# Kernel tuning notes

Measured on AMD Instinct MI355X. Metric: run time of the kernel, lower is better.

Reference implementation:

```python
import jax, jax.numpy as jnp
import numpy as np

D_MODEL = 1024
N_HEADS = 16
D_HEAD = D_MODEL // N_HEADS


def setup_inputs() -> dict:
    key = jax.random.key(0)
    ks = jax.random.split(key, 5)
    B, T = 2, 2048
    x = jax.random.normal(ks[0], (B, T, D_MODEL), dtype=jnp.float32)
    s = 1.0 / np.sqrt(D_MODEL)
    W_qkv = jax.random.normal(ks[1], (D_MODEL, 3 * D_MODEL), dtype=jnp.float32) * s
    b_qkv = jnp.zeros((3 * D_MODEL,), dtype=jnp.float32)
    W_proj = jax.random.normal(ks[2], (D_MODEL, D_MODEL), dtype=jnp.float32) * s
    b_proj = jnp.zeros((D_MODEL,), dtype=jnp.float32)
    return {"x": x, "W_qkv": W_qkv, "b_qkv": b_qkv, "W_proj": W_proj, "b_proj": b_proj}


def reference(x, W_qkv, b_qkv, W_proj, b_proj):
    B, T, C = x.shape
    qkv = x @ W_qkv + b_qkv                      # [B,T,3C]
    q, k, v = jnp.split(qkv, 3, axis=-1)
    # [B,T,C] -> [B,H,T,Dh]
    def to_heads(t):
        return t.reshape(B, T, N_HEADS, D_HEAD).transpose(0, 2, 1, 3)
    q, k, v = to_heads(q), to_heads(k), to_heads(v)
    scale = 1.0 / np.sqrt(D_HEAD).astype(np.float32)
    scores = jnp.einsum('bhqd,bhkd->bhqk', q, k) * scale  # [B,H,T,T]
    causal = jnp.tril(jnp.ones((T, T), dtype=bool))
    scores = jnp.where(causal, scores, -jnp.inf)
    attn = jax.nn.softmax(scores, axis=-1)
    out = jnp.einsum('bhqk,bhkd->bhqd', attn, v)          # [B,H,T,Dh]
    out = out.transpose(0, 2, 1, 3).reshape(B, T, C)
    return out @ W_proj + b_proj
```

## Files before the change

kernel.cpp:

```cpp
#include <hip/hip_runtime.h>
#include <hip/hip_bf16.h>
#include <cstdint>


using u16 = unsigned short;
using u32 = unsigned int;

typedef __bf16 bf16x8 __attribute__((ext_vector_type(8)));
typedef float f32x4 __attribute__((ext_vector_type(4)));

#define AS1 __attribute__((address_space(1)))
#define AS3 __attribute__((address_space(3)))

__device__ __forceinline__ u16 f2bf(float f) {
  u32 u = __float_as_uint(f);
  u += 0x7fffu + ((u >> 16) & 1u);
  return (u16)(u >> 16);
}
__device__ __forceinline__ u32 pack2bf(float a, float b) {
  u32 ua = __float_as_uint(a) + 0x8000u;
  u32 ub = __float_as_uint(b) + 0x8000u;
  return (ua >> 16) | (ub & 0xffff0000u);
}

__global__ __launch_bounds__(256) void prep(const float* __restrict__ x,
                                            u16* __restrict__ xb,
                                            const float* __restrict__ W0,
                                            u16* __restrict__ T0,
                                            const float* __restrict__ W1,
                                            u16* __restrict__ T1) {
  const int bx = blockIdx.x;
  const int tid = threadIdx.x;
  if (bx < 4096) {
    const int i = bx * 256 + tid;
    float4 v = ((const float4*)x)[i];
    ushort4 o;
    o.x = f2bf(v.x); o.y = f2bf(v.y); o.z = f2bf(v.z); o.w = f2bf(v.w);
    ((ushort4*)xb)[i] = o;
    return;
  }
  __shared__ float t[32][33];
  const int idx = bx - 4096;
  const int bxx = idx & 127, by = idx >> 7;
  const float* W; u16* Wt; int N, n0;
  if (bxx < 96) { W = W0; Wt = T0; N = 3072; n0 = bxx * 32; }
  else          { W = W1; Wt = T1; N = 1024; n0 = (bxx - 96) * 32; }
  const int k0 = by * 32;
  const int tx = tid & 31, ty = tid >> 5;
#pragma unroll
  for (int i = 0; i < 4; ++i)
    t[ty + i * 8][tx] = W[(size_t)(k0 + ty + i * 8) * N + n0 + tx];
  __syncthreads();
#pragma unroll
  for (int i = 0; i < 4; ++i)
    Wt[(size_t)(n0 + ty + i * 8) * 1024 + k0 + tx] = f2bf(t[tx][ty + i * 8]);
}

#define MFMA16 __builtin_amdgcn_mfma_f32_16x16x32_bf16

__global__ __launch_bounds__(512, 2) void gemm_qkv(const u16* __restrict__ A,
                                                   const u16* __restrict__ Bt,
                                                   const float* __restrict__ bias,
                                                   u16* __restrict__ qb,
                                                   u16* __restrict__ KF,
                                                   u16* __restrict__ VF,
                                                   float sc_val) {
  constexpr int NT = 16;
  __shared__ __align__(16) u16 sm[2 * 4 * 8192];

  const int tid  = threadIdx.x;
  const int lane = tid & 63;
  const int w    = tid >> 6;
  const int quad = lane >> 4;
  const int l15  = lane & 15;

  const int bid = blockIdx.x;
  const int xcd = bid & 7, c = bid >> 3;
  const int mt = (xcd >> 1) * 4 + (c & 3);
  const int nt = (xcd & 1) * 6 + (c >> 2);
  const int bm = mt * 256, bn = nt * 256;

  const int wr = (w >> 2) * 128;
  const int wc = (w & 3) * 64;

  const int rowS = w * 8 + (lane >> 3);
  const int scol = (((lane & 7) ^ (lane >> 3)) << 3);

#define STAGE(matp, rowbase, ldsoff, ktile)                                     \
  do {                                                                          \
    const u16* _s = (matp) + ((size_t)((rowbase) + rowS) << 10) +               \
                    ((ktile) << 6) + scol;                                      \
    u16* _d = sm + (ldsoff) + (w << 9);                                         \
    __builtin_amdgcn_global_load_lds((AS1 const void*)_s, (AS3 void*)_d,        \
                                     16, 0, 0);                                 \
    __builtin_amdgcn_global_load_lds((AS1 const void*)(_s + (64 << 10)),        \
                                     (AS3 void*)(_d + 4096), 16, 0, 0);         \
  } while (0)

  const int raoff = (wr >> 7) * 8192;
  const int rboff = (2 + (wc >> 7)) * 8192;
  const int av0 = l15 * 64 + ((quad ^ (l15 & 7)) << 3);
  const int av1 = l15 * 64 + (((4 + quad) ^ (l15 & 7)) << 3);
  const int bv0 = ((wc & 64) + l15) * 64 + ((quad ^ (l15 & 7)) << 3);
  const int bv1 = ((wc & 64) + l15) * 64 + (((4 + quad) ^ (l15 & 7)) << 3);

  STAGE(A,  bm,       0 * 8192, 0);
  STAGE(A,  bm + 128, 1 * 8192, 0);
  STAGE(Bt, bn,       2 * 8192, 0);
  STAGE(Bt, bn + 128, 3 * 8192, 0);
  STAGE(Bt, bn,       32768 + 2 * 8192, 1);
  STAGE(A,  bm,       32768 + 0 * 8192, 1);
  STAGE(A,  bm + 128, 32768 + 1 * 8192, 1);
  asm volatile("s_waitcnt vmcnt(6)" ::: "memory");
  __builtin_amdgcn_s_barrier();

  f32x4 acc[8][4] = {};
  bf16x8 a[4][2], b[4][2];

#pragma unroll 2
  for (int kt = 0; kt < NT; ++kt) {
    const int bo  = (kt & 1) * 32768;
    const int nbo = bo ^ 32768;
    const u16* smA = sm + bo + raoff;
    const u16* smB = sm + bo + rboff;

#pragma unroll
    for (int mi = 0; mi < 4; ++mi) {
      a[mi][0] = *(const bf16x8*)(smA + mi * 1024 + av0);
      a[mi][1] = *(const bf16x8*)(smA + mi * 1024 + av1);
    }
#pragma unroll
    for (int ni = 0; ni < 2; ++ni) {
      b[ni][0] = *(const bf16x8*)(smB + ni * 1024 + bv0);
      b[ni][1] = *(const bf16x8*)(smB + ni * 1024 + bv1);
    }
    if (kt + 1 < NT) STAGE(Bt, bn + 128, nbo + 3 * 8192, kt + 1);
    __builtin_amdgcn_s_barrier();
    asm volatile("s_waitcnt lgkmcnt(0)" ::: "memory");
    __builtin_amdgcn_s_setprio(1);
#pragma unroll
    for (int mi = 0; mi < 4; ++mi)
#pragma unroll
      for (int ni = 0; ni < 2; ++ni) {
        acc[mi][ni] = MFMA16(a[mi][0], b[ni][0], acc[mi][ni], 0, 0, 0);
        acc[mi][ni] = MFMA16(a[mi][1], b[ni][1], acc[mi][ni], 0, 0, 0);
      }
    __builtin_amdgcn_s_setprio(0);
    __builtin_amdgcn_s_barrier();

#pragma unroll
    for (int ni = 2; ni < 4; ++ni) {
      b[ni][0] = *(const bf16x8*)(smB + ni * 1024 + bv0);
      b[ni][1] = *(const bf16x8*)(smB + ni * 1024 + bv1);
    }
    __builtin_amdgcn_s_barrier();
    asm volatile("s_waitcnt lgkmcnt(0)" ::: "memory");
    __builtin_amdgcn_s_setprio(1);
#pragma unroll
    for (int mi = 0; mi < 4; ++mi)
#pragma unroll
      for (int ni = 2; ni < 4; ++ni) {
        acc[mi][ni] = MFMA16(a[mi][0], b[ni][0], acc[mi][ni], 0, 0, 0);
        acc[mi][ni] = MFMA16(a[mi][1], b[ni][1], acc[mi][ni], 0, 0, 0);
      }
    __builtin_amdgcn_s_setprio(0);
    __builtin_amdgcn_s_barrier();

#pragma unroll
    for (int mi = 0; mi < 4; ++mi) {
      a[mi][0] = *(const bf16x8*)(smA + (4 + mi) * 1024 + av0);
      a[mi][1] = *(const bf16x8*)(smA + (4 + mi) * 1024 + av1);
    }
    if (kt + 2 < NT) STAGE(Bt, bn, bo + 2 * 8192, kt + 2);
    __builtin_amdgcn_s_barrier();
    asm volatile("s_waitcnt lgkmcnt(0)" ::: "memory");
    __builtin_amdgcn_s_setprio(1);
#pragma unroll
    for (int mi = 0; mi < 4; ++mi)
#pragma unroll
      for (int ni = 2; ni < 4; ++ni) {
        acc[4 + mi][ni] = MFMA16(a[mi][0], b[ni][0], acc[4 + mi][ni], 0, 0, 0);
        acc[4 + mi][ni] = MFMA16(a[mi][1], b[ni][1], acc[4 + mi][ni], 0, 0, 0);
      }
    __builtin_amdgcn_s_setprio(0);
    __builtin_amdgcn_s_barrier();

    if (kt + 2 < NT) {
      STAGE(A, bm,       bo + 0 * 8192, kt + 2);
      STAGE(A, bm + 128, bo + 1 * 8192, kt + 2);
    }
    __builtin_amdgcn_s_barrier();
    __builtin_amdgcn_s_setprio(1);
#pragma unroll
    for (int mi = 0; mi < 4; ++mi)
#pragma unroll
      for (int ni = 0; ni < 2; ++ni) {
        acc[4 + mi][ni] = MFMA16(a[mi][0], b[ni][0], acc[4 + mi][ni], 0, 0, 0);
        acc[4 + mi][ni] = MFMA16(a[mi][1], b[ni][1], acc[4 + mi][ni], 0, 0, 0);
      }
    __builtin_amdgcn_s_setprio(0);
    if (kt + 2 < NT)
      asm volatile("s_waitcnt vmcnt(6)" ::: "memory");
    else
      asm volatile("s_waitcnt vmcnt(0)" ::: "memory");
    __builtin_amdgcn_s_barrier();
  }
#undef STAGE

  const int crow0 = bm + wr + (quad << 2);
  const int ccol0 = bn + wc + l15;
  if (bn < 1024) {
#pragma unroll
    for (int ni = 0; ni < 4; ++ni) {
      const int n = ccol0 + ni * 16;
      const float bv = bias[n];
#pragma unroll
      for (int mi = 0; mi < 8; ++mi) {
        const int m0 = crow0 + mi * 16;
#pragma unroll
        for (int r = 0; r < 4; ++r)
          qb[(size_t)(m0 + r) * 1024 + n] = f2bf((acc[mi][ni][r] + bv) * sc_val);
      }
    }
  } else if (bn < 2048) {
#pragma unroll
    for (int ni = 0; ni < 4; ++ni) {
      const int n  = ccol0 + ni * 16;
      const int hk = (n - 1024) >> 6;
      const int d  = (n - 1024) & 63;
      const int hh = d >> 5, qd = (d >> 3) & 3, j = d & 7;
      const float bv = bias[n];
#pragma unroll
      for (int mi = 0; mi < 8; ++mi) {
#pragma unroll
        for (int r = 0; r < 4; ++r) {
          const int t  = crow0 + mi * 16 + r;
          const int bb = t >> 11, tt = t & 2047;
          const int kt = tt >> 6, mm = (tt >> 4) & 3, l = tt & 15;
          KF[((size_t)((bb * 16 + hk) * 32 + kt) * 8 + mm * 2 + hh) * 512 +
             (qd * 16 + l) * 8 + j] = f2bf(acc[mi][ni][r] + bv);
        }
      }
    }
  } else {
#pragma unroll
    for (int ni = 0; ni < 4; ++ni) {
      const int n  = ccol0 + ni * 16;
      const int hv = (n - 2048) >> 6;
      const int d  = (n - 2048) & 63;
      const int di = d >> 4, l = d & 15;
      const float bv = bias[n];
#pragma unroll
      for (int mi = 0; mi < 8; ++mi) {
#pragma unroll
        for (int r = 0; r < 4; ++r) {
          const int t  = crow0 + mi * 16 + r;
          const int bb = t >> 11, tt = t & 2047;
          const int kt = tt >> 6, to = tt & 63;
          const int mq = to >> 4, qd2 = (to >> 2) & 3, rr = to & 3;
          const int hh = mq >> 1, j = (mq & 1) * 4 + rr;
          VF[((size_t)((bb * 16 + hv) * 32 + kt) * 8 + hh * 4 + di) * 512 +
             (qd2 * 16 + l) * 8 + j] = f2bf(acc[mi][ni][r] + bv);
        }
      }
    }
  }
}

__global__ __launch_bounds__(256) void gemm_proj(const u16* __restrict__ A,
                                                 const u16* __restrict__ Bt,
                                                 const float* __restrict__ bias,
                                                 float* __restrict__ C) {
  constexpr int BM = 128, BN = 64, BK = 32;
  constexpr int K = 1024, N = 1024;
  __shared__ __align__(16) u16 lA[BM * BK];
  __shared__ __align__(16) u16 lB[BN * BK];
  const int tid  = threadIdx.x;
  const int lane = tid & 63;
  const int wave = tid >> 6;
  const int bm = blockIdx.x * BM;
  const int bn = blockIdx.y * BN;
  const int wr = wave * 32;

  f32x4 acc[2][4] = {};

  const int f0 = (wave << 10) + (lane << 4);
  const int f1 = f0 + 4096;
  const int ar0 = f0 >> 6, ac0 = (f0 & 63) >> 1;
  const int ar1 = f1 >> 6, ac1 = (f1 & 63) >> 1;

  const int arow = wr + (lane & 15);
  const int brow = (lane & 15);
  const int kk   = (lane >> 4) << 3;

  for (int k0 = 0; k0 < K; k0 += BK) {
    __builtin_amdgcn_global_load_lds((AS1 const void*)(A + (size_t)(bm + ar0) * K + k0 + ac0),
                                     (AS3 void*)(lA + (wave << 9)), 16, 0, 0);
    __builtin_amdgcn_global_load_lds((AS1 const void*)(A + (size_t)(bm + ar1) * K + k0 + ac1),
                                     (AS3 void*)(lA + ((wave + 4) << 9)), 16, 0, 0);
    __builtin_amdgcn_global_load_lds((AS1 const void*)(Bt + (size_t)(bn + ar0) * K + k0 + ac0),
                                     (AS3 void*)(lB + (wave << 9)), 16, 0, 0);
    __syncthreads();

    bf16x8 af[2], bfr[4];
#pragma unroll
    for (int mi = 0; mi < 2; ++mi)
      af[mi] = *(const bf16x8*)&lA[(arow + mi * 16) * BK + kk];
#pragma unroll
    for (int ni = 0; ni < 4; ++ni)
      bfr[ni] = *(const bf16x8*)&lB[(brow + ni * 16) * BK + kk];
#pragma unroll
    for (int mi = 0; mi < 2; ++mi)
#pragma unroll
      for (int ni = 0; ni < 4; ++ni)
        acc[mi][ni] = __builtin_amdgcn_mfma_f32_16x16x32_bf16(af[mi], bfr[ni],
                                                              acc[mi][ni], 0, 0, 0);
    __syncthreads();
  }

  const int crow0 = bm + wr + ((lane >> 4) << 2);
  const int ccol0 = bn + (lane & 15);
#pragma unroll
  for (int ni = 0; ni < 4; ++ni) {
    const int n = ccol0 + ni * 16;
    const float bv = bias[n];
#pragma unroll
    for (int mi = 0; mi < 2; ++mi) {
      const int m0 = crow0 + mi * 16;
#pragma unroll
      for (int r = 0; r < 4; ++r)
        C[(size_t)(m0 + r) * N + n] = acc[mi][ni][r] + bv;
    }
  }
}

__global__ __launch_bounds__(256) void attn_bal(const u16* __restrict__ qb,
                                                const u16* __restrict__ KF,
                                                const u16* __restrict__ VF,
                                                u16* __restrict__ out) {
  const int u  = blockIdx.x;
  const int bh = blockIdx.y;
  const int b = bh >> 4, h = bh & 15;
  const int tid = threadIdx.x;
  const int lane = tid & 63;
  const int w    = tid >> 6;
  const int quad = lane >> 4;
  const int l15  = lane & 15;
  const int g32 = (w & 1) ? (63 - u) : u;
  const int par = w >> 1;
  const int q0 = g32 * 32;
  const int ktmax = g32 >> 1;

  __shared__ float CB[2][64][35];

  const u16* qbase = qb + (size_t)b * 2048 * 1024 + h * 64;
  bf16x8 qf[2][2];
#pragma unroll
  for (int g = 0; g < 2; ++g)
#pragma unroll
    for (int hh = 0; hh < 2; ++hh)
      qf[g][hh] = *(const bf16x8*)(qbase + (size_t)(q0 + g * 16 + l15) * 1024 +
                                   hh * 32 + quad * 8);

  const size_t fb = (size_t)bh * 32 * 4096 + lane * 8;
  const u16* kfb = KF + fb;
  const u16* vfb = VF + fb;

  f32x4 accO[2][4] = {};
  float lrow[2] = {0.f, 0.f};

  bf16x8 kcur[4][2];
  {
    const u16* kp = kfb + (size_t)par * 4096;
#pragma unroll
    for (int m = 0; m < 4; ++m)
#pragma unroll
      for (int hh = 0; hh < 2; ++hh)
        kcur[m][hh] = *(const bf16x8*)(kp + (m * 2 + hh) * 512);
  }

  for (int kt = par; kt <= ktmax; kt += 2) {
    const u16* vp = vfb + (size_t)kt * 4096;
    bf16x8 vfr[2][4];
#pragma unroll
    for (int hh = 0; hh < 2; ++hh)
#pragma unroll
      for (int di = 0; di < 4; ++di)
        vfr[hh][di] = *(const bf16x8*)(vp + (hh * 4 + di) * 512);
    const int ktn = (kt + 2 <= ktmax) ? kt + 2 : ktmax;
    const u16* kpn = kfb + (size_t)ktn * 4096;
    bf16x8 knx[4][2];
#pragma unroll
    for (int m = 0; m < 4; ++m)
#pragma unroll
      for (int hh = 0; hh < 2; ++hh)
        knx[m][hh] = *(const bf16x8*)(kpn + (m * 2 + hh) * 512);

    const bool diag = (kt == ktmax);
    bf16x8 ap[2][2];
#pragma unroll
    for (int g = 0; g < 2; ++g) {
      f32x4 sT[4] = {};
#pragma unroll
      for (int m = 0; m < 4; ++m) {
        sT[m] = __builtin_amdgcn_mfma_f32_16x16x32_bf16(kcur[m][0], qf[g][0], sT[m], 0, 0, 0);
        sT[m] = __builtin_amdgcn_mfma_f32_16x16x32_bf16(kcur[m][1], qf[g][1], sT[m], 0, 0, 0);
      }
      float pv[4][4];
      if (diag) {
        const int qgl = q0 + g * 16 + l15;
#pragma unroll
        for (int m = 0; m < 4; ++m)
#pragma unroll
          for (int r = 0; r < 4; ++r) {
            const bool msk = (kt * 64 + m * 16 + quad * 4 + r) > qgl;
            pv[m][r] = msk ? 0.f : __builtin_amdgcn_exp2f(sT[m][r]);
          }
      } else {
#pragma unroll
        for (int m = 0; m < 4; ++m)
#pragma unroll
          for (int r = 0; r < 4; ++r)
            pv[m][r] = __builtin_amdgcn_exp2f(sT[m][r]);
      }
      const float s0 = (pv[0][0] + pv[0][1]) + (pv[0][2] + pv[0][3]);
      const float s1 = (pv[1][0] + pv[1][1]) + (pv[1][2] + pv[1][3]);
      const float s2 = (pv[2][0] + pv[2][1]) + (pv[2][2] + pv[2][3]);
      const float s3 = (pv[3][0] + pv[3][1]) + (pv[3][2] + pv[3][3]);
      lrow[g] += (s0 + s1) + (s2 + s3);

      union { u32 u4[4]; bf16x8 v; } t0, t1;
      t0.u4[0] = pack2bf(pv[0][0], pv[0][1]);
      t0.u4[1] = pack2bf(pv[0][2], pv[0][3]);
      t0.u4[2] = pack2bf(pv[1][0], pv[1][1]);
      t0.u4[3] = pack2bf(pv[1][2], pv[1][3]);
      t1.u4[0] = pack2bf(pv[2][0], pv[2][1]);
      t1.u4[1] = pack2bf(pv[2][2], pv[2][3]);
      t1.u4[2] = pack2bf(pv[3][0], pv[3][1]);
      t1.u4[3] = pack2bf(pv[3][2], pv[3][3]);
      ap[g][0] = t0.v;
      ap[g][1] = t1.v;
    }

#pragma unroll
    for (int hh = 0; hh < 2; ++hh)
#pragma unroll
      for (int di = 0; di < 4; ++di) {
        bf16x8 bv = vfr[hh][di];
#pragma unroll
        for (int g = 0; g < 2; ++g)
          accO[g][di] = __builtin_amdgcn_mfma_f32_16x16x32_bf16(ap[g][hh], bv,
                                                               accO[g][di], 0, 0, 0);
      }

#pragma unroll
    for (int m = 0; m < 4; ++m)
#pragma unroll
      for (int hh = 0; hh < 2; ++hh)
        kcur[m][hh] = knx[m][hh];
  }

  if (par) {
    float* cb = CB[w & 1][lane];
#pragma unroll
    for (int g = 0; g < 2; ++g)
#pragma unroll
      for (int di = 0; di < 4; ++di)
#pragma unroll
        for (int r = 0; r < 4; ++r)
          cb[g * 16 + di * 4 + r] = accO[g][di][r];
    cb[32] = lrow[0];
    cb[33] = lrow[1];
  }
  __syncthreads();
  if (!par) {
    const float* cb = CB[w & 1][lane];
#pragma unroll
    for (int g = 0; g < 2; ++g)
#pragma unroll
      for (int di = 0; di < 4; ++di)
#pragma unroll
        for (int r = 0; r < 4; ++r)
          accO[g][di][r] += cb[g * 16 + di * 4 + r];
    lrow[0] += cb[32];
    lrow[1] += cb[33];
#pragma unroll
    for (int g = 0; g < 2; ++g) {
      lrow[g] += __shfl_xor(lrow[g], 16);
      lrow[g] += __shfl_xor(lrow[g], 32);
    }

#pragma unroll
    for (int g = 0; g < 2; ++g)
#pragma unroll
      for (int r = 0; r < 4; ++r) {
        const float lv = __shfl(lrow[g], quad * 4 + r);
        const float inv = 1.f / lv;
        const int q = q0 + g * 16 + quad * 4 + r;
        u16* op = out + (size_t)(b * 2048 + q) * 1024 + h * 64 + l15;
#pragma unroll
        for (int di = 0; di < 4; ++di)
          op[di * 16] = f2bf(accO[g][di][r] * inv);
      }
  }
}

extern "C" void kernel_launch(void* const* d_in, const int* in_sizes, int n_in,
                              void* d_out, int out_size, void* d_ws, size_t ws_size,
                              hipStream_t stream) {
  const float* x     = (const float*)d_in[0];
  const float* Wqkv  = (const float*)d_in[1];
  const float* bqkv  = (const float*)d_in[2];
  const float* Wproj = (const float*)d_in[3];
  const float* bproj = (const float*)d_in[4];
  float* out = (float*)d_out;

  char* ws = (char*)d_ws;
  u16* xb     = (u16*)(ws);
  u16* wqkvT  = (u16*)(ws + 8388608);
  u16* wprojT = (u16*)(ws + 14680064);
  u16* qb     = (u16*)(ws + 16777216);
  u16* KF     = (u16*)(ws + 25165824);
  u16* VF     = (u16*)(ws + 33554432);
  u16* att    = (u16*)(ws + 41943040);

  constexpr float cs = 0.18033688011f;

  prep<<<8192, 256, 0, stream>>>(x, xb, Wqkv, wqkvT, Wproj, wprojT);

  gemm_qkv<<<dim3(192), 512, 0, stream>>>(xb, wqkvT, bqkv, qb, KF, VF, cs);

  attn_bal<<<dim3(32, 32), 256, 0, stream>>>(qb, KF, VF, att);

  gemm_proj<<<dim3(32, 16), 256, 0, stream>>>(att, wprojT, bproj, out);
}
```

Measured before the change: 176.6 us.

## Retile QKV GEMM to 256x192 blocks and remap attention grid for XCD locality

The QKV projection GEMM changes from 256x256 tiles (192 blocks) to 256x192 tiles (256 blocks), so the grid matches the 256 CUs of the device. Each wave now computes a 128x48 sub-tile, and the LDS staging, double-buffer pipeline and epilogue routing to Q/K/V are restructured to match. The attention launch becomes a flat 1D grid whose block index is decoded so that blocks for the same (batch, head) land on the same XCD, which is meant to improve L2 reuse of K and V. The trade-off is less data reuse per tile and a per-column branch in the epilogue, since Q, K and V boundaries now fall mid-tile.

```diff
diff --git a/kernel.cpp b/kernel.cpp
--- a/kernel.cpp
+++ b/kernel.cpp
@@ -66,7 +66,8 @@
                                                    u16* __restrict__ VF,
                                                    float sc_val) {
   constexpr int NT = 16;
-  __shared__ __align__(16) u16 sm[2 * 4 * 8192];
+  constexpr int BUFO = 7 * 4096;
+  __shared__ __align__(16) u16 sm[2 * BUFO];
 
   const int tid  = threadIdx.x;
   const int lane = tid & 63;
@@ -77,64 +78,68 @@
   const int bid = blockIdx.x;
   const int xcd = bid & 7, c = bid >> 3;
   const int mt = (xcd >> 1) * 4 + (c & 3);
-  const int nt = (xcd & 1) * 6 + (c >> 2);
-  const int bm = mt * 256, bn = nt * 256;
+  const int nt = (xcd & 1) * 8 + (c >> 2);
+  const int bm = mt * 256, bn = nt * 192;
 
   const int wr = (w >> 2) * 128;
-  const int wc = (w & 3) * 64;
-
-  const int rowS = w * 8 + (lane >> 3);
-  const int scol = (((lane & 7) ^ (lane >> 3)) << 3);
-
-#define STAGE(matp, rowbase, ldsoff, ktile)                                     \
-  do {                                                                          \
-    const u16* _s = (matp) + ((size_t)((rowbase) + rowS) << 10) +               \
-                    ((ktile) << 6) + scol;                                      \
-    u16* _d = sm + (ldsoff) + (w << 9);                                         \
-    __builtin_amdgcn_global_load_lds((AS1 const void*)_s, (AS3 void*)_d,        \
-                                     16, 0, 0);                                 \
-    __builtin_amdgcn_global_load_lds((AS1 const void*)(_s + (64 << 10)),        \
-                                     (AS3 void*)(_d + 4096), 16, 0, 0);         \
-  } while (0)
-
-  const int raoff = (wr >> 7) * 8192;
-  const int rboff = (2 + (wc >> 7)) * 8192;
-  const int av0 = l15 * 64 + ((quad ^ (l15 & 7)) << 3);
-  const int av1 = l15 * 64 + (((4 + quad) ^ (l15 & 7)) << 3);
-  const int bv0 = ((wc & 64) + l15) * 64 + ((quad ^ (l15 & 7)) << 3);
-  const int bv1 = ((wc & 64) + l15) * 64 + (((4 + quad) ^ (l15 & 7)) << 3);
-
-  STAGE(A,  bm,       0 * 8192, 0);
-  STAGE(A,  bm + 128, 1 * 8192, 0);
-  STAGE(Bt, bn,       2 * 8192, 0);
-  STAGE(Bt, bn + 128, 3 * 8192, 0);
-  STAGE(Bt, bn,       32768 + 2 * 8192, 1);
-  STAGE(A,  bm,       32768 + 0 * 8192, 1);
-  STAGE(A,  bm + 128, 32768 + 1 * 8192, 1);
-  asm volatile("s_waitcnt vmcnt(6)" ::: "memory");
+  const int wc = (w & 3) * 48;
+
+  const int srow = tid >> 3;
+  const int scol = (((tid & 7) ^ ((tid >> 3) & 7)) << 3);
+
+#define STAGEA(ch, ktile, bufo)                                                 \
+  __builtin_amdgcn_global_load_lds(                                             \
+      (AS1 const void*)(A + (size_t)(bm + (ch) * 64 + srow) * 1024 +            \
+                        ((ktile) << 6) + scol),                                 \
+      (AS3 void*)(sm + (bufo) + (ch) * 4096 + tid * 8), 16, 0, 0)
+#define STAGEB(ch, ktile, bufo)                                                 \
+  __builtin_amdgcn_global_load_lds(                                             \
+      (AS1 const void*)(Bt + (size_t)(bn + (ch) * 64 + srow) * 1024 +           \
+                        ((ktile) << 6) + scol),                                 \
+      (AS3 void*)(sm + (bufo) + (4 + (ch)) * 4096 + tid * 8), 16, 0, 0)
+
+  const int ca = (w >> 2) * 2;
+  int abase_lo[4], abase_hi[4], bbase[3];
+#pragma unroll
+  for (int mi = 0; mi < 4; ++mi) {
+    abase_lo[mi] = (ca + 0) * 4096 + (mi * 16 + l15) * 64;
+    abase_hi[mi] = (ca + 1) * 4096 + (mi * 16 + l15) * 64;
+  }
+#pragma unroll
+  for (int ni = 0; ni < 3; ++ni) {
+    const int rb = wc + ni * 16 + l15;
+    bbase[ni] = (4 + (rb >> 6)) * 4096 + (rb & 63) * 64;
+  }
+  const int sw0 = ((quad ^ (l15 & 7)) << 3);
+  const int sw1 = sw0 ^ 32;
+
+  STAGEA(0, 0, 0); STAGEA(1, 0, 0); STAGEA(2, 0, 0); STAGEA(3, 0, 0);
+  STAGEB(0, 0, 0); STAGEB(1, 0, 0); STAGEB(2, 0, 0);
+  STAGEB(0, 1, BUFO); STAGEB(1, 1, BUFO);
+  STAGEB(2, 1, BUFO); STAGEA(0, 1, BUFO); STAGEA(1, 1, BUFO);
+  asm volatile("s_waitcnt vmcnt(5)" ::: "memory");
   __builtin_amdgcn_s_barrier();
 
-  f32x4 acc[8][4] = {};
-  bf16x8 a[4][2], b[4][2];
+  f32x4 acc[8][3] = {};
+  bf16x8 alo[4][2], ahi[4][2], b[3][2];
 
 #pragma unroll 2
-  for (int kt = 0; kt < NT; ++kt) {
-    const int bo  = (kt & 1) * 32768;
-    const int nbo = bo ^ 32768;
-    const u16* smA = sm + bo + raoff;
-    const u16* smB = sm + bo + rboff;
+  for (int j = 0; j < NT; ++j) {
+    const int bo  = (j & 1) * BUFO;
+    const int nbo = bo ^ BUFO;
+    const u16* smb = sm + bo;
 
 #pragma unroll
     for (int mi = 0; mi < 4; ++mi) {
-      a[mi][0] = *(const bf16x8*)(smA + mi * 1024 + av0);
-      a[mi][1] = *(const bf16x8*)(smA + mi * 1024 + av1);
+      alo[mi][0] = *(const bf16x8*)(smb + abase_lo[mi] + sw0);
+      alo[mi][1] = *(const bf16x8*)(smb + abase_lo[mi] + sw1);
     }
 #pragma unroll
     for (int ni = 0; ni < 2; ++ni) {
-      b[ni][0] = *(const bf16x8*)(smB + ni * 1024 + bv0);
-      b[ni][1] = *(const bf16x8*)(smB + ni * 1024 + bv1);
-    }
-    if (kt + 1 < NT) STAGE(Bt, bn + 128, nbo + 3 * 8192, kt + 1);
+      b[ni][0] = *(const bf16x8*)(smb + bbase[ni] + sw0);
+      b[ni][1] = *(const bf16x8*)(smb + bbase[ni] + sw1);
+    }
+    if (j + 1 < NT) { STAGEA(2, j + 1, nbo); STAGEA(3, j + 1, nbo); }
     __builtin_amdgcn_s_barrier();
     asm volatile("s_waitcnt lgkmcnt(0)" ::: "memory");
     __builtin_amdgcn_s_setprio(1);
@@ -142,78 +147,60 @@
     for (int mi = 0; mi < 4; ++mi)
 #pragma unroll
       for (int ni = 0; ni < 2; ++ni) {
-        acc[mi][ni] = MFMA16(a[mi][0], b[ni][0], acc[mi][ni], 0, 0, 0);
-        acc[mi][ni] = MFMA16(a[mi][1], b[ni][1], acc[mi][ni], 0, 0, 0);
+        acc[mi][ni] = MFMA16(alo[mi][0], b[ni][0], acc[mi][ni], 0, 0, 0);
+        acc[mi][ni] = MFMA16(alo[mi][1], b[ni][1], acc[mi][ni], 0, 0, 0);
       }
     __builtin_amdgcn_s_setprio(0);
     __builtin_amdgcn_s_barrier();
 
 #pragma unroll
-    for (int ni = 2; ni < 4; ++ni) {
-      b[ni][0] = *(const bf16x8*)(smB + ni * 1024 + bv0);
-      b[ni][1] = *(const bf16x8*)(smB + ni * 1024 + bv1);
-    }
+    for (int mi = 0; mi < 4; ++mi) {
+      ahi[mi][0] = *(const bf16x8*)(smb + abase_hi[mi] + sw0);
+      ahi[mi][1] = *(const bf16x8*)(smb + abase_hi[mi] + sw1);
+    }
+    b[2][0] = *(const bf16x8*)(smb + bbase[2] + sw0);
+    b[2][1] = *(const bf16x8*)(smb + bbase[2] + sw1);
+    if (j + 2 < NT) { STAGEB(0, j + 2, bo); STAGEB(1, j + 2, bo); }
     __builtin_amdgcn_s_barrier();
     asm volatile("s_waitcnt lgkmcnt(0)" ::: "memory");
     __builtin_amdgcn_s_setprio(1);
 #pragma unroll
-    for (int mi = 0; mi < 4; ++mi)
-#pragma unroll
-      for (int ni = 2; ni < 4; ++ni) {
-        acc[mi][ni] = MFMA16(a[mi][0], b[ni][0], acc[mi][ni], 0, 0, 0);
-        acc[mi][ni] = MFMA16(a[mi][1], b[ni][1], acc[mi][ni], 0, 0, 0);
-      }
+    for (int mi = 0; mi < 4; ++mi) {
+      acc[mi][2] = MFMA16(alo[mi][0], b[2][0], acc[mi][2], 0, 0, 0);
+      acc[mi][2] = MFMA16(alo[mi][1], b[2][1], acc[mi][2], 0, 0, 0);
+      acc[4 + mi][0] = MFMA16(ahi[mi][0], b[0][0], acc[4 + mi][0], 0, 0, 0);
+      acc[4 + mi][0] = MFMA16(ahi[mi][1], b[0][1], acc[4 + mi][0], 0, 0, 0);
+    }
     __builtin_amdgcn_s_setprio(0);
     __builtin_amdgcn_s_barrier();
 
-#pragma unroll
-    for (int mi = 0; mi < 4; ++mi) {
-      a[mi][0] = *(const bf16x8*)(smA + (4 + mi) * 1024 + av0);
-      a[mi][1] = *(const bf16x8*)(smA + (4 + mi) * 1024 + av1);
-    }
-    if (kt + 2 < NT) STAGE(Bt, bn, bo + 2 * 8192, kt + 2);
-    __builtin_amdgcn_s_barrier();
-    asm volatile("s_waitcnt lgkmcnt(0)" ::: "memory");
-    __builtin_amdgcn_s_setprio(1);
-#pragma unroll
-    for (int mi = 0; mi < 4; ++mi)
-#pragma unroll
-      for (int ni = 2; ni < 4; ++ni) {
-        acc[4 + mi][ni] = MFMA16(a[mi][0], b[ni][0], acc[4 + mi][ni], 0, 0, 0);
-        acc[4 + mi][ni] = MFMA16(a[mi][1], b[ni][1], acc[4 + mi][ni], 0, 0, 0);
-      }
-    __builtin_amdgcn_s_setprio(0);
-    __builtin_amdgcn_s_barrier();
-
-    if (kt + 2 < NT) {
-      STAGE(A, bm,       bo + 0 * 8192, kt + 2);
-      STAGE(A, bm + 128, bo + 1 * 8192, kt + 2);
-    }
+    if (j + 2 < NT) { STAGEB(2, j + 2, bo); STAGEA(0, j + 2, bo); STAGEA(1, j + 2, bo); }
     __builtin_amdgcn_s_barrier();
     __builtin_amdgcn_s_setprio(1);
 #pragma unroll
     for (int mi = 0; mi < 4; ++mi)
 #pragma unroll
-      for (int ni = 0; ni < 2; ++ni) {
-        acc[4 + mi][ni] = MFMA16(a[mi][0], b[ni][0], acc[4 + mi][ni], 0, 0, 0);
-        acc[4 + mi][ni] = MFMA16(a[mi][1], b[ni][1], acc[4 + mi][ni], 0, 0, 0);
+      for (int ni = 1; ni < 3; ++ni) {
+        acc[4 + mi][ni] = MFMA16(ahi[mi][0], b[ni][0], acc[4 + mi][ni], 0, 0, 0);
+        acc[4 + mi][ni] = MFMA16(ahi[mi][1], b[ni][1], acc[4 + mi][ni], 0, 0, 0);
       }
     __builtin_amdgcn_s_setprio(0);
-    if (kt + 2 < NT)
-      asm volatile("s_waitcnt vmcnt(6)" ::: "memory");
+    if (j + 2 < NT)
+      asm volatile("s_waitcnt vmcnt(5)" ::: "memory");
     else
       asm volatile("s_waitcnt vmcnt(0)" ::: "memory");
     __builtin_amdgcn_s_barrier();
   }
-#undef STAGE
+#undef STAGEA
+#undef STAGEB
 
   const int crow0 = bm + wr + (quad << 2);
   const int ccol0 = bn + wc + l15;
-  if (bn < 1024) {
-#pragma unroll
-    for (int ni = 0; ni < 4; ++ni) {
-      const int n = ccol0 + ni * 16;
-      const float bv = bias[n];
+#pragma unroll
+  for (int ni = 0; ni < 3; ++ni) {
+    const int n = ccol0 + ni * 16;
+    const float bv = bias[n];
+    if (n < 1024) {
 #pragma unroll
       for (int mi = 0; mi < 8; ++mi) {
         const int m0 = crow0 + mi * 16;
@@ -221,15 +208,10 @@
         for (int r = 0; r < 4; ++r)
           qb[(size_t)(m0 + r) * 1024 + n] = f2bf((acc[mi][ni][r] + bv) * sc_val);
       }
-    }
-  } else if (bn < 2048) {
-#pragma unroll
-    for (int ni = 0; ni < 4; ++ni) {
-      const int n  = ccol0 + ni * 16;
+    } else if (n < 2048) {
       const int hk = (n - 1024) >> 6;
       const int d  = (n - 1024) & 63;
-      const int hh = d >> 5, qd = (d >> 3) & 3, j = d & 7;
-      const float bv = bias[n];
+      const int hh = d >> 5, qd = (d >> 3) & 3, jj = d & 7;
 #pragma unroll
       for (int mi = 0; mi < 8; ++mi) {
 #pragma unroll
@@ -238,18 +220,13 @@
           const int bb = t >> 11, tt = t & 2047;
           const int kt = tt >> 6, mm = (tt >> 4) & 3, l = tt & 15;
           KF[((size_t)((bb * 16 + hk) * 32 + kt) * 8 + mm * 2 + hh) * 512 +
-             (qd * 16 + l) * 8 + j] = f2bf(acc[mi][ni][r] + bv);
+             (qd * 16 + l) * 8 + jj] = f2bf(acc[mi][ni][r] + bv);
         }
       }
-    }
-  } else {
-#pragma unroll
-    for (int ni = 0; ni < 4; ++ni) {
-      const int n  = ccol0 + ni * 16;
+    } else {
       const int hv = (n - 2048) >> 6;
       const int d  = (n - 2048) & 63;
       const int di = d >> 4, l = d & 15;
-      const float bv = bias[n];
 #pragma unroll
       for (int mi = 0; mi < 8; ++mi) {
 #pragma unroll
@@ -258,9 +235,9 @@
           const int bb = t >> 11, tt = t & 2047;
           const int kt = tt >> 6, to = tt & 63;
           const int mq = to >> 4, qd2 = (to >> 2) & 3, rr = to & 3;
-          const int hh = mq >> 1, j = (mq & 1) * 4 + rr;
+          const int hh = mq >> 1, jj = (mq & 1) * 4 + rr;
           VF[((size_t)((bb * 16 + hv) * 32 + kt) * 8 + hh * 4 + di) * 512 +
-             (qd2 * 16 + l) * 8 + j] = f2bf(acc[mi][ni][r] + bv);
+             (qd2 * 16 + l) * 8 + jj] = f2bf(acc[mi][ni][r] + bv);
         }
       }
     }
@@ -338,8 +315,9 @@
                                                 const u16* __restrict__ KF,
                                                 const u16* __restrict__ VF,
                                                 u16* __restrict__ out) {
-  const int u  = blockIdx.x;
-  const int bh = blockIdx.y;
+  const int f  = blockIdx.x;
+  const int u  = (f >> 3) & 31;
+  const int bh = (f & 7) | ((f >> 8) << 3);
   const int b = bh >> 4, h = bh & 15;
   const int tid = threadIdx.x;
   const int lane = tid & 63;
@@ -528,9 +506,9 @@
 
   prep<<<8192, 256, 0, stream>>>(x, xb, Wqkv, wqkvT, Wproj, wprojT);
 
-  gemm_qkv<<<dim3(192), 512, 0, stream>>>(xb, wqkvT, bqkv, qb, KF, VF, cs);
-
-  attn_bal<<<dim3(32, 32), 256, 0, stream>>>(qb, KF, VF, att);
+  gemm_qkv<<<dim3(256), 512, 0, stream>>>(xb, wqkvT, bqkv, qb, KF, VF, cs);
+
+  attn_bal<<<dim3(1024), 256, 0, stream>>>(qb, KF, VF, att);
 
   gemm_proj<<<dim3(32, 16), 256, 0, stream>>>(att, wprojT, bproj, out);
 }
```

New measurement: 168.1 us. 4.8% less time.
